# Kernel tuning notes

Hardware: AMD Instinct MI355X
Metric: run time of the kernel (lower is better)

Reference implementation:

```python
import jax, jax.numpy as jnp
import numpy as np

EPS = 1e-12  # torch F.normalize eps

def _l2norm(v, axis):
    n = jnp.sqrt(jnp.sum(v * v, axis=axis, keepdims=True))
    return v / jnp.maximum(n, EPS)

def setup_inputs() -> dict:
    key = jax.random.key(0)
    k1, k2, k3 = jax.random.split(key, 3)
    N, C, H, W, K = 64, 512, 32, 32, 64
    x = jax.random.normal(k1, (N, C, H, W), dtype=jnp.float32)
    conv_w = jax.random.normal(k2, (K, C), dtype=jnp.float32) * 0.05
    centroids = jax.random.uniform(k3, (K, C), dtype=jnp.float32)
    return {"x": x, "conv_w": conv_w, "centroids": centroids}

def reference(x, conv_w, centroids):
    N, C, H, W = x.shape
    K = centroids.shape[0]
    # descriptor-wise L2 normalization over channel dim
    x = _l2norm(x, axis=1)
    xf = x.reshape(N, C, H * W)                       # (N, C, S)
    # 1x1 conv (no bias) == per-pixel matmul, then softmax over clusters
    logits = jnp.einsum('kc,ncs->nks', conv_w, xf)    # (N, K, S)
    a = jax.nn.softmax(logits, axis=1)                # softmax over clusters
    # vlad[n,k,:] = sum_s a[n,k,s] * (x[n,:,s] - centroid[k])
    # = (a @ x^T) - centroid * sum_s a   -- two GEMM-like ops, no (N,K,C,S) tensor
    vlad = jnp.einsum('nks,ncs->nkc', a, xf) - a.sum(axis=-1)[..., None] * centroids[None, :, :]
    # intra-normalization per cluster, flatten, global L2 norm
    vlad = _l2norm(vlad, axis=2)
    vlad = vlad.reshape(N, K * C)
    vlad = _l2norm(vlad, axis=1)
    return vlad
```

## Files before the change

kernel.cpp:

```cpp
#include <hip/hip_runtime.h>
#include <hip/hip_bf16.h>
#include <math.h>

#define EPSF 1e-12f

typedef __attribute__((ext_vector_type(8))) short bf16x8;
typedef __attribute__((ext_vector_type(4))) float f32x4;
typedef __attribute__((ext_vector_type(4))) short short4v;
typedef __attribute__((ext_vector_type(4))) unsigned short ushort4v;

static __device__ __forceinline__ short f2bf(float f) {
  union { __hip_bfloat16 h; short s; } u;
  u.h = __float2bfloat16(f);
  return u.s;
}

__global__ __launch_bounds__(256) void k2_mfma(
    const float* __restrict__ x, const float* __restrict__ w,
    unsigned short* __restrict__ ap, float* __restrict__ suma) {
  __shared__ __align__(16) float xf[64][70];
  __shared__ __align__(16) short wb[64][72];
  __shared__ __align__(16) float red[4][64];
  __shared__ float invs[64];
  __shared__ float gmaxs[64];
  __shared__ float gsums[64];

  const int n = blockIdx.y;
  const int s0 = blockIdx.x << 6;
  const int t = threadIdx.x;
  const int lane = t & 63;
  const int wid = t >> 6;
  const int col = t & 15;
  const int quad = (t >> 4) & 3;
  const int cr = t >> 4;
  const int sg = t & 15;

  f32x4 acc[4] = {{0,0,0,0},{0,0,0,0},{0,0,0,0},{0,0,0,0}};
  float ssq0 = 0.f, ssq1 = 0.f, ssq2 = 0.f, ssq3 = 0.f;

  for (int c0 = 0; c0 < 512; c0 += 64) {
#pragma unroll
    for (int p = 0; p < 4; ++p) {
      int c = cr + (p << 4);
      float4 g = *(const float4*)&x[((size_t)((n << 9) + c0 + c) << 10) + s0 + (sg << 2)];
      float2 glo; glo.x = g.x; glo.y = g.y;
      float2 ghi; ghi.x = g.z; ghi.y = g.w;
      *(float2*)&xf[c][sg << 2] = glo;
      *(float2*)&xf[c][(sg << 2) + 2] = ghi;
      ssq0 = fmaf(g.x, g.x, ssq0); ssq1 = fmaf(g.y, g.y, ssq1);
      ssq2 = fmaf(g.z, g.z, ssq2); ssq3 = fmaf(g.w, g.w, ssq3);
      float4 gw = *(const float4*)&w[(c << 9) + c0 + (sg << 2)];
      short4v hw; hw.x = f2bf(gw.x); hw.y = f2bf(gw.y); hw.z = f2bf(gw.z); hw.w = f2bf(gw.w);
      *(short4v*)&wb[c][sg << 2] = hw;
    }
    __syncthreads();
#pragma unroll
    for (int cc = 0; cc < 64; cc += 32) {
      bf16x8 af = *(const bf16x8*)&wb[(wid << 4) + col][cc + (quad << 3)];
      int cb = cc + (quad << 3);
#pragma unroll
      for (int sgr = 0; sgr < 4; ++sgr) {
        int sc = (sgr << 4) + col;
        bf16x8 bfr;
#pragma unroll
        for (int j = 0; j < 8; ++j) bfr[j] = f2bf(xf[cb + j][sc]);
        acc[sgr] = __builtin_amdgcn_mfma_f32_16x16x32_bf16(af, bfr, acc[sgr], 0, 0, 0);
      }
    }
    __syncthreads();
  }

  ssq0 += __shfl_xor(ssq0, 16, 64); ssq0 += __shfl_xor(ssq0, 32, 64);
  ssq1 += __shfl_xor(ssq1, 16, 64); ssq1 += __shfl_xor(ssq1, 32, 64);
  ssq2 += __shfl_xor(ssq2, 16, 64); ssq2 += __shfl_xor(ssq2, 32, 64);
  ssq3 += __shfl_xor(ssq3, 16, 64); ssq3 += __shfl_xor(ssq3, 32, 64);
  if (lane < 16) {
    float4 v; v.x = ssq0; v.y = ssq1; v.z = ssq2; v.w = ssq3;
    *(float4*)&red[wid][sg << 2] = v;
  }
  __syncthreads();
  if (t < 64) {
    float tot = red[0][t] + red[1][t] + red[2][t] + red[3][t];
    invs[t] = 1.0f / fmaxf(sqrtf(tot), EPSF);
  }
  __syncthreads();

  float li[4];
#pragma unroll
  for (int sgr = 0; sgr < 4; ++sgr) li[sgr] = invs[(sgr << 4) + col];
  float le[4][4];
#pragma unroll
  for (int sgr = 0; sgr < 4; ++sgr)
#pragma unroll
    for (int r = 0; r < 4; ++r) le[sgr][r] = acc[sgr][r] * li[sgr];

  float mx[4];
#pragma unroll
  for (int sgr = 0; sgr < 4; ++sgr) {
    float m = fmaxf(fmaxf(le[sgr][0], le[sgr][1]), fmaxf(le[sgr][2], le[sgr][3]));
    m = fmaxf(m, __shfl_xor(m, 16, 64));
    m = fmaxf(m, __shfl_xor(m, 32, 64));
    mx[sgr] = m;
  }
  if (lane < 16) {
#pragma unroll
    for (int sgr = 0; sgr < 4; ++sgr) red[wid][(sgr << 4) + sg] = mx[sgr];
  }
  __syncthreads();
  if (t < 64)
    gmaxs[t] = fmaxf(fmaxf(red[0][t], red[1][t]), fmaxf(red[2][t], red[3][t]));
  __syncthreads();

  float ps[4];
#pragma unroll
  for (int sgr = 0; sgr < 4; ++sgr) {
    float gm = gmaxs[(sgr << 4) + col];
    float p = 0.f;
#pragma unroll
    for (int r = 0; r < 4; ++r) {
      float e = __expf(le[sgr][r] - gm);
      le[sgr][r] = e;
      p += e;
    }
    p += __shfl_xor(p, 16, 64);
    p += __shfl_xor(p, 32, 64);
    ps[sgr] = p;
  }
  if (lane < 16) {
#pragma unroll
    for (int sgr = 0; sgr < 4; ++sgr) red[wid][(sgr << 4) + sg] = ps[sgr];
  }
  __syncthreads();
  if (t < 64) gsums[t] = red[0][t] + red[1][t] + red[2][t] + red[3][t];
  __syncthreads();

  float sk[4] = {0.f, 0.f, 0.f, 0.f};
#pragma unroll
  for (int sgr = 0; sgr < 4; ++sgr) {
    float rinv = 1.0f / gsums[(sgr << 4) + col];
#pragma unroll
    for (int r = 0; r < 4; ++r) {
      float av = le[sgr][r] * rinv;
      sk[r] += av;
      float apv = av * li[sgr];
      int k = (wid << 4) + (quad << 2) + r;
      ap[((size_t)((n << 6) + k) << 10) + s0 + (sgr << 4) + col] =
          (unsigned short)f2bf(apv);
    }
  }
#pragma unroll
  for (int r = 0; r < 4; ++r) {
    sk[r] += __shfl_xor(sk[r], 1, 64);
    sk[r] += __shfl_xor(sk[r], 2, 64);
    sk[r] += __shfl_xor(sk[r], 4, 64);
    sk[r] += __shfl_xor(sk[r], 8, 64);
  }
  if (col == 0) {
#pragma unroll
    for (int r = 0; r < 4; ++r)
      atomicAdd(&suma[(n << 6) + (wid << 4) + (quad << 2) + r], sk[r]);
  }
}

#define K3_LOADT(GX0, GX1, GA0, GA1, TI)                                       \
  do {                                                                         \
    const int so_ = (TI) << 6;                                                 \
    GX0 = *(const float4*)(xbase + so_);                                       \
    GX1 = *(const float4*)(xbase + so_ + 32);                                  \
    GA0 = *(const bf16x8*)(abase + so_);                                       \
    GA1 = *(const bf16x8*)(abase + so_ + 32);                                  \
  } while (0)

#define K3_WRITET(GX0, GX1, GA0, GA1, XB, AT)                                  \
  do {                                                                         \
    short4v h0, h1;                                                            \
    h0.x = f2bf(GX0.x); h0.y = f2bf(GX0.y); h0.z = f2bf(GX0.z); h0.w = f2bf(GX0.w); \
    h1.x = f2bf(GX1.x); h1.y = f2bf(GX1.y); h1.z = f2bf(GX1.z); h1.w = f2bf(GX1.w); \
    *(short4v*)&XB[t >> 3][(t & 7) << 2] = h0;                                 \
    *(short4v*)&XB[t >> 3][((t & 7) << 2) + 32] = h1;                          \
    *(bf16x8*)&AT[t >> 2][(t & 3) << 3] = GA0;                                 \
    *(bf16x8*)&AT[t >> 2][((t & 3) << 3) + 32] = GA1;                          \
  } while (0)

#define K3_MFMAT(XB, AT)                                                       \
  do {                                                                         \
    _Pragma("unroll") for (int ss = 0; ss < 64; ss += 32) {                    \
      bf16x8 af = *(const bf16x8*)&XB[cb + col][ss + (quad << 3)];             \
      _Pragma("unroll") for (int kt = 0; kt < 2; ++kt) {                       \
        bf16x8 bfr = *(const bf16x8*)&AT[kb + (kt << 4) + col][ss + (quad << 3)]; \
        acc[kt] = __builtin_amdgcn_mfma_f32_16x16x32_bf16(af, bfr, acc[kt], 0, 0, 0); \
      }                                                                        \
    }                                                                          \
  } while (0)

__global__ __launch_bounds__(256, 4) void k3_mfma(
    const float* __restrict__ x, const unsigned short* __restrict__ ap,
    const float* __restrict__ cent, const float* __restrict__ suma,
    float* __restrict__ out, float* __restrict__ rnorm2) {
  __shared__ __align__(16) char sm[27648];
  short (*xb0)[72] = reinterpret_cast<short(*)[72]>(sm);
  short (*at0)[72] = reinterpret_cast<short(*)[72]>(sm + 4608);
  short (*xb1)[72] = reinterpret_cast<short(*)[72]>(sm + 13824);
  short (*at1)[72] = reinterpret_cast<short(*)[72]>(sm + 18432);
  float (*lt)[36] = reinterpret_cast<float(*)[36]>(sm);

  const int n = blockIdx.x;
  const int c0 = blockIdx.y << 5;
  const int t = threadIdx.x;
  const int lane = t & 63;
  const int wid = t >> 6;
  const int col = t & 15;
  const int quad = (t >> 4) & 3;
  const int sg = t & 15;
  const int cb = (wid & 1) << 4;
  const int kb = (wid >> 1) << 5;

  f32x4 acc[2] = {{0, 0, 0, 0}, {0, 0, 0, 0}};

  const float* xbase = &x[((size_t)((n << 9) + c0 + (t >> 3)) << 10) + ((t & 7) << 2)];
  const unsigned short* abase = &ap[((size_t)((n << 6) + (t >> 2)) << 10) + ((t & 3) << 3)];

  float4 xA0, xA1, xB0, xB1;
  bf16x8 aA0, aA1, aB0, aB1;

  K3_LOADT(xA0, xA1, aA0, aA1, 0);
  K3_WRITET(xA0, xA1, aA0, aA1, xb0, at0);
  K3_LOADT(xB0, xB1, aB0, aB1, 1);
  __syncthreads();

#pragma unroll 1
  for (int it = 0; it < 16; it += 2) {
    const bool last = (it == 14);
    K3_WRITET(xB0, xB1, aB0, aB1, xb1, at1);
    if (!last) K3_LOADT(xA0, xA1, aA0, aA1, it + 2);
    K3_MFMAT(xb0, at0);
    __syncthreads();
    if (!last) {
      K3_WRITET(xA0, xA1, aA0, aA1, xb0, at0);
      K3_LOADT(xB0, xB1, aB0, aB1, it + 3);
    }
    K3_MFMAT(xb1, at1);
    __syncthreads();
  }

  const float sa0 = suma[(n << 6) + kb + col];
  const float sa1 = suma[(n << 6) + kb + 16 + col];
  const int crow = cb + (quad << 2);
  const int k0 = kb + col;
  const int k1 = kb + 16 + col;
  float r2_0 = 0.f, r2_1 = 0.f;
#pragma unroll
  for (int r = 0; r < 4; ++r) {
    int c = crow + r;
    float ce0 = cent[(k0 << 9) + c0 + c];
    float v0 = acc[0][r] - sa0 * ce0;
    r2_0 = fmaf(v0, v0, r2_0);
    lt[k0][c] = v0;
    float ce1 = cent[(k1 << 9) + c0 + c];
    float v1 = acc[1][r] - sa1 * ce1;
    r2_1 = fmaf(v1, v1, r2_1);
    lt[k1][c] = v1;
  }
  r2_0 += __shfl_xor(r2_0, 16, 64); r2_0 += __shfl_xor(r2_0, 32, 64);
  r2_1 += __shfl_xor(r2_1, 16, 64); r2_1 += __shfl_xor(r2_1, 32, 64);
  if (lane < 16) {
    atomicAdd(&rnorm2[(n << 6) + kb + sg], r2_0);
    atomicAdd(&rnorm2[(n << 6) + kb + 16 + sg], r2_1);
  }
  __syncthreads();
#pragma unroll
  for (int u = 0; u < 2; ++u) {
    int kk = t >> 2;
    int c = ((t & 3) << 2) + (u << 4);
    float4 v = *(const float4*)&lt[kk][c];
    *(float4*)&out[((size_t)((n << 6) + kk) << 9) + c0 + c] = v;
  }
}

__global__ __launch_bounds__(256) void k5_scale(const float* __restrict__ vlad,
                                                const float* __restrict__ rnorm2,
                                                float* __restrict__ out) {
  __shared__ float gsh;
  const int b = blockIdx.x;
  const int t = threadIdx.x;
  const int n = b >> 5;
  if (t < 64) {
    float rn = sqrtf(rnorm2[(n << 6) + t]);
    float nr = rn / fmaxf(rn, EPSF);
    float g = nr * nr;
#pragma unroll
    for (int off = 32; off > 0; off >>= 1) g += __shfl_xor(g, off, 64);
    if (t == 0) gsh = g;
  }
  __syncthreads();
  const float ginv = 1.0f / fmaxf(sqrtf(gsh), EPSF);
  const int idx = (b << 8) + t;
  const int kg = idx >> 7;
  float rn = sqrtf(rnorm2[kg]);
  float f = (1.0f / fmaxf(rn, EPSF)) * ginv;
  float4 v = ((const float4*)vlad)[idx];
  float4 o;
  o.x = v.x * f; o.y = v.y * f; o.z = v.z * f; o.w = v.w * f;
  ((float4*)out)[idx] = o;
}

extern "C" void kernel_launch(void* const* d_in, const int* in_sizes, int n_in,
                              void* d_out, int out_size, void* d_ws, size_t ws_size,
                              hipStream_t stream) {
  (void)in_sizes; (void)n_in; (void)out_size; (void)ws_size;
  const float* x = (const float*)d_in[0];
  const float* w = (const float*)d_in[1];
  const float* cent = (const float*)d_in[2];
  float* out = (float*)d_out;

  float* ws = (float*)d_ws;
  float* suma = ws;
  float* rnorm2 = ws + 4096;
  unsigned short* ap = (unsigned short*)(ws + 12288);

  hipMemsetAsync(ws, 0, 8192 * sizeof(float), stream);
  k2_mfma<<<dim3(16, 64), 256, 0, stream>>>(x, w, ap, suma);
  k3_mfma<<<dim3(64, 16), 256, 0, stream>>>(x, ap, cent, suma, out, rnorm2);
  k5_scale<<<2048, 256, 0, stream>>>(out, rnorm2, out);
}
```

Baseline: 228.3 us.

## Switch k2 logits GEMM to 32x32x16 MFMA with 2x2 wave tiling

The logits kernel now has each of the four waves compute a 32x32 (cluster x pixel) tile with the 32x32x16 bf16 MFMA, replacing a 16-row band across all 64 pixels built from four 16x16x32 MFMAs. This reduces redundant LDS reads and bf16 conversions of the x tile, since each wave now converts only its 32-pixel half. The softmax reductions are reworked for the new accumulator layout: cross-wave max and sum now combine pairs of waves, and per-cluster sums use a deeper shuffle before the atomics. The trade-off is more shuffles per output element and a different LDS access pattern.

```diff
diff --git a/kernel.cpp b/kernel.cpp
--- a/kernel.cpp
+++ b/kernel.cpp
@@ -6,6 +6,7 @@
 
 typedef __attribute__((ext_vector_type(8))) short bf16x8;
 typedef __attribute__((ext_vector_type(4))) float f32x4;
+typedef __attribute__((ext_vector_type(16))) float f32x16;
 typedef __attribute__((ext_vector_type(4))) short short4v;
 typedef __attribute__((ext_vector_type(4))) unsigned short ushort4v;
 
@@ -30,12 +31,14 @@
   const int t = threadIdx.x;
   const int lane = t & 63;
   const int wid = t >> 6;
-  const int col = t & 15;
-  const int quad = (t >> 4) & 3;
+  const int l31 = t & 31;
+  const int half = lane >> 5;
+  const int kband = (wid & 1) << 5;
+  const int sband = (wid >> 1) << 5;
   const int cr = t >> 4;
   const int sg = t & 15;
 
-  f32x4 acc[4] = {{0,0,0,0},{0,0,0,0},{0,0,0,0},{0,0,0,0}};
+  f32x16 acc = {0,0,0,0,0,0,0,0,0,0,0,0,0,0,0,0};
   float ssq0 = 0.f, ssq1 = 0.f, ssq2 = 0.f, ssq3 = 0.f;
 
   for (int c0 = 0; c0 < 512; c0 += 64) {
@@ -55,17 +58,13 @@
     }
     __syncthreads();
 #pragma unroll
-    for (int cc = 0; cc < 64; cc += 32) {
-      bf16x8 af = *(const bf16x8*)&wb[(wid << 4) + col][cc + (quad << 3)];
-      int cb = cc + (quad << 3);
-#pragma unroll
-      for (int sgr = 0; sgr < 4; ++sgr) {
-        int sc = (sgr << 4) + col;
-        bf16x8 bfr;
-#pragma unroll
-        for (int j = 0; j < 8; ++j) bfr[j] = f2bf(xf[cb + j][sc]);
-        acc[sgr] = __builtin_amdgcn_mfma_f32_16x16x32_bf16(af, bfr, acc[sgr], 0, 0, 0);
-      }
+    for (int ks = 0; ks < 4; ++ks) {
+      const int cb = (ks << 4) + (half << 3);
+      bf16x8 af = *(const bf16x8*)&wb[kband + l31][cb];
+      bf16x8 bfr;
+#pragma unroll
+      for (int j = 0; j < 8; ++j) bfr[j] = f2bf(xf[cb + j][sband + l31]);
+      acc = __builtin_amdgcn_mfma_f32_32x32x16_bf16(af, bfr, acc, 0, 0, 0);
     }
     __syncthreads();
   }
@@ -85,80 +84,63 @@
   }
   __syncthreads();
 
-  float li[4];
-#pragma unroll
-  for (int sgr = 0; sgr < 4; ++sgr) li[sgr] = invs[(sgr << 4) + col];
-  float le[4][4];
-#pragma unroll
-  for (int sgr = 0; sgr < 4; ++sgr)
-#pragma unroll
-    for (int r = 0; r < 4; ++r) le[sgr][r] = acc[sgr][r] * li[sgr];
-
-  float mx[4];
-#pragma unroll
-  for (int sgr = 0; sgr < 4; ++sgr) {
-    float m = fmaxf(fmaxf(le[sgr][0], le[sgr][1]), fmaxf(le[sgr][2], le[sgr][3]));
-    m = fmaxf(m, __shfl_xor(m, 16, 64));
-    m = fmaxf(m, __shfl_xor(m, 32, 64));
-    mx[sgr] = m;
-  }
-  if (lane < 16) {
-#pragma unroll
-    for (int sgr = 0; sgr < 4; ++sgr) red[wid][(sgr << 4) + sg] = mx[sgr];
-  }
-  __syncthreads();
-  if (t < 64)
-    gmaxs[t] = fmaxf(fmaxf(red[0][t], red[1][t]), fmaxf(red[2][t], red[3][t]));
-  __syncthreads();
-
-  float ps[4];
-#pragma unroll
-  for (int sgr = 0; sgr < 4; ++sgr) {
-    float gm = gmaxs[(sgr << 4) + col];
-    float p = 0.f;
-#pragma unroll
-    for (int r = 0; r < 4; ++r) {
-      float e = __expf(le[sgr][r] - gm);
-      le[sgr][r] = e;
-      p += e;
+  const int sl = sband + l31;
+  const float li = invs[sl];
+  float le[16];
+#pragma unroll
+  for (int r = 0; r < 16; ++r) le[r] = acc[r] * li;
+
+  float m = le[0];
+#pragma unroll
+  for (int r = 1; r < 16; ++r) m = fmaxf(m, le[r]);
+  m = fmaxf(m, __shfl_xor(m, 32, 64));
+  if (lane < 32) red[wid][l31] = m;
+  __syncthreads();
+  if (t < 64) {
+    int w0 = (t >> 5) << 1;
+    gmaxs[t] = fmaxf(red[w0][t & 31], red[w0 + 1][t & 31]);
+  }
+  __syncthreads();
+
+  const float gm = gmaxs[sl];
+  float p = 0.f;
+#pragma unroll
+  for (int r = 0; r < 16; ++r) {
+    float e = __expf(le[r] - gm);
+    le[r] = e;
+    p += e;
+  }
+  p += __shfl_xor(p, 32, 64);
+  if (lane < 32) red[wid][l31] = p;
+  __syncthreads();
+  if (t < 64) {
+    int w0 = (t >> 5) << 1;
+    gsums[t] = red[w0][t & 31] + red[w0 + 1][t & 31];
+  }
+  __syncthreads();
+
+  const float rinv = 1.0f / gsums[sl];
+  const int kb2 = kband + (half << 2);
+#pragma unroll
+  for (int r = 0; r < 16; ++r) {
+    float av = le[r] * rinv;
+    le[r] = av;
+    float apv = av * li;
+    int k = kb2 + (r & 3) + ((r >> 2) << 3);
+    ap[((size_t)((n << 6) + k) << 10) + s0 + sl] = (unsigned short)f2bf(apv);
+  }
+#pragma unroll
+  for (int r = 0; r < 16; ++r) {
+    float v = le[r];
+    v += __shfl_xor(v, 1, 64);
+    v += __shfl_xor(v, 2, 64);
+    v += __shfl_xor(v, 4, 64);
+    v += __shfl_xor(v, 8, 64);
+    v += __shfl_xor(v, 16, 64);
+    if (l31 == 0) {
+      int k = kb2 + (r & 3) + ((r >> 2) << 3);
+      atomicAdd(&suma[(n << 6) + k], v);
     }
-    p += __shfl_xor(p, 16, 64);
-    p += __shfl_xor(p, 32, 64);
-    ps[sgr] = p;
-  }
-  if (lane < 16) {
-#pragma unroll
-    for (int sgr = 0; sgr < 4; ++sgr) red[wid][(sgr << 4) + sg] = ps[sgr];
-  }
-  __syncthreads();
-  if (t < 64) gsums[t] = red[0][t] + red[1][t] + red[2][t] + red[3][t];
-  __syncthreads();
-
-  float sk[4] = {0.f, 0.f, 0.f, 0.f};
-#pragma unroll
-  for (int sgr = 0; sgr < 4; ++sgr) {
-    float rinv = 1.0f / gsums[(sgr << 4) + col];
-#pragma unroll
-    for (int r = 0; r < 4; ++r) {
-      float av = le[sgr][r] * rinv;
-      sk[r] += av;
-      float apv = av * li[sgr];
-      int k = (wid << 4) + (quad << 2) + r;
-      ap[((size_t)((n << 6) + k) << 10) + s0 + (sgr << 4) + col] =
-          (unsigned short)f2bf(apv);
-    }
-  }
-#pragma unroll
-  for (int r = 0; r < 4; ++r) {
-    sk[r] += __shfl_xor(sk[r], 1, 64);
-    sk[r] += __shfl_xor(sk[r], 2, 64);
-    sk[r] += __shfl_xor(sk[r], 4, 64);
-    sk[r] += __shfl_xor(sk[r], 8, 64);
-  }
-  if (col == 0) {
-#pragma unroll
-    for (int r = 0; r < 4; ++r)
-      atomicAdd(&suma[(n << 6) + (wid << 4) + (quad << 2) + r], sk[r]);
   }
 }
 
```

New measurement: 228.1 us (median of 2 runs). Within noise of the previous version (-0.1%).
